# Performance work log

Measured on AMD Instinct MI355X. Metric: run time of the kernel, lower is better.

## Reference

```python
import jax, jax.numpy as jnp
import numpy as np

# sRGB -> XYZ matrix (skimage/CIE, D65 observer 2deg)
_RGB2XYZ = jnp.array([[0.412453, 0.357580, 0.180423],
                      [0.212671, 0.715160, 0.072169],
                      [0.019334, 0.119193, 0.950227]], dtype=jnp.float32)
_WHITE_D65 = jnp.array([0.95047, 1.0, 1.08883], dtype=jnp.float32)


def _srgb_to_linear(c):
    # inverse sRGB gamma
    return jnp.where(c > 0.04045, ((c + 0.055) / 1.055) ** 2.4, c / 12.92)


def _xyz_f(t):
    # CIE Lab nonlinearity
    eps = 0.008856
    return jnp.where(t > eps, jnp.cbrt(t), 7.787 * t + 16.0 / 116.0)


def _rgb2lab(img):
    # img: [..., H, W, 3] sRGB in [0,1]
    lin = _srgb_to_linear(img)
    xyz = jnp.einsum('...c,dc->...d', lin, _RGB2XYZ) / _WHITE_D65
    f = _xyz_f(xyz)
    fx, fy, fz = f[..., 0], f[..., 1], f[..., 2]
    L = 116.0 * fy - 16.0
    a = 500.0 * (fx - fy)
    b = 200.0 * (fy - fz)
    return jnp.stack([L, a, b], axis=-1)


def setup_inputs() -> dict:
    key = jax.random.key(0)
    x = jax.random.uniform(key, (512, 128, 128, 3), dtype=jnp.float32)
    return {"x": x}


def reference(x) -> jnp.ndarray:
    lab = _rgb2lab(x)                       # [B,H,W,3]
    L = lab[..., 0]
    # per-image min-max normalize L channel (reduce over H,W)
    Lmin = jnp.min(L, axis=(1, 2), keepdims=True)
    Lmax = jnp.max(L, axis=(1, 2), keepdims=True)
    L01 = (L - Lmin) / (Lmax - Lmin)
    ab01 = (lab[..., 1:] + 128.0) / 255.0
    out = jnp.concatenate([L01[..., None], ab01], axis=-1)
    return jax.lax.stop_gradient(out).astype(jnp.float32)
```

## Files before the change

### kernel.cpp

```cpp
#include <hip/hip_runtime.h>

#define TPB 1024

typedef __fp16 half2_t __attribute__((ext_vector_type(2)));

__device__ __forceinline__ float fexp2(float x) { return __builtin_amdgcn_exp2f(x); }
__device__ __forceinline__ float flog2(float x) { return __builtin_amdgcn_logf(x); }

__device__ __forceinline__ float s2lin(float c) {
    float p = fexp2(flog2((c + 0.055f) * (1.0f / 1.055f)) * 2.4f);
    float l = c * (1.0f / 12.92f);
    return c > 0.04045f ? p : l;
}

__device__ __forceinline__ float labf(float t) {
    float p = fexp2(flog2(t) * (1.0f / 3.0f));
    float l = 7.787f * t + (16.0f / 116.0f);
    return t > 0.008856f ? p : l;
}

__device__ __forceinline__ void px(float r, float g, float b,
                                   float& L, float& a01, float& b01) {
    float lr = s2lin(r), lg = s2lin(g), lb = s2lin(b);
    float X = 0.43395300f * lr + 0.37621900f * lg + 0.18982460f * lb;
    float Y = 0.21267100f * lr + 0.71516000f * lg + 0.07216900f * lb;
    float Z = 0.01775660f * lr + 0.10946970f * lg + 0.87270740f * lb;
    float fx = labf(X), fy = labf(Y), fz = labf(Z);
    L   = 116.0f * fy - 16.0f;
    a01 = (500.0f * (fx - fy) + 128.0f) * (1.0f / 255.0f);
    b01 = (200.0f * (fy - fz) + 128.0f) * (1.0f / 255.0f);
}

__global__ __launch_bounds__(TPB, 8) void lab_norm_kernel(
        const float* __restrict__ x, float* __restrict__ out) {
    __shared__ float lds[12288];
    __shared__ float smin[16], smax[16];

    const int img = blockIdx.x;
    const size_t ibase = (size_t)img * 49152;
    const int t = threadIdx.x;
    float4* const l4 = (float4*)lds;

    float   Lr[16];
    half2_t AB[16];
    float lmin = 3.4e38f, lmax = -3.4e38f;

#pragma unroll
    for (int g = 0; g < 4; ++g) {
        const float4* __restrict__ in4 = (const float4*)(x + ibase) + g * 3072;
        l4[t]        = in4[t];
        l4[t + 1024] = in4[t + 1024];
        l4[t + 2048] = in4[t + 2048];
        __syncthreads();
#pragma unroll
        for (int j = 0; j < 4; ++j) {
            int p3 = 3 * t + j * 3072;
            float r = lds[p3], gg = lds[p3 + 1], b = lds[p3 + 2];
            float L, a01, b01;
            px(r, gg, b, L, a01, b01);
            lmin = fminf(lmin, L);
            lmax = fmaxf(lmax, L);
            Lr[g * 4 + j] = L;
            AB[g * 4 + j] = __builtin_amdgcn_cvt_pkrtz(a01, b01);
        }
        __syncthreads();
    }

#pragma unroll
    for (int m = 32; m >= 1; m >>= 1) {
        lmin = fminf(lmin, __shfl_xor(lmin, m, 64));
        lmax = fmaxf(lmax, __shfl_xor(lmax, m, 64));
    }
    int wid = t >> 6;
    if ((t & 63) == 0) { smin[wid] = lmin; smax[wid] = lmax; }
    __syncthreads();
    float bmin = smin[0], bmax = smax[0];
#pragma unroll
    for (int i = 1; i < 16; ++i) {
        bmin = fminf(bmin, smin[i]);
        bmax = fmaxf(bmax, smax[i]);
    }
    float s = 1.0f / (bmax - bmin);

#pragma unroll
    for (int g = 0; g < 4; ++g) {
#pragma unroll
        for (int j = 0; j < 4; ++j) {
            int p3 = 3 * t + j * 3072;
            half2_t hv = AB[g * 4 + j];
            lds[p3]     = (Lr[g * 4 + j] - bmin) * s;
            lds[p3 + 1] = (float)hv.x;
            lds[p3 + 2] = (float)hv.y;
        }
        __syncthreads();
        float4* __restrict__ o4 = (float4*)(out + ibase) + g * 3072;
        o4[t]        = l4[t];
        o4[t + 1024] = l4[t + 1024];
        o4[t + 2048] = l4[t + 2048];
        __syncthreads();
    }
}

extern "C" void kernel_launch(void* const* d_in, const int* in_sizes, int n_in,
                              void* d_out, int out_size, void* d_ws, size_t ws_size,
                              hipStream_t stream) {
    (void)in_sizes; (void)n_in; (void)out_size; (void)d_ws; (void)ws_size;
    const float* x = (const float*)d_in[0];
    float* out = (float*)d_out;
    lab_norm_kernel<<<512, TPB, 0, stream>>>(x, out);
}
```

Before: 202.6 us.

## Split into pack and unpack kernels with compact per-pixel workspace encoding

Replaces the single one-block-per-image kernel with two launches of 4096 small blocks, eight per image. The first kernel computes Lab per pixel, records per-block partial min and max of L (max taken as min of 100-L), and packs each pixel into 32 bits: a and b quantized to 8 bits, L stored as fp16. The second kernel combines the partial extrema, unpacks, normalizes L and writes the output. Spreading the work across many more blocks is meant to raise occupancy and memory-level parallelism, at the cost of an extra workspace round trip and lossy quantization of a/b and L. A fallback pair of kernels writes raw output and rescales it in place when the workspace is too small.

```diff
diff --git a/kernel.cpp b/kernel.cpp
--- a/kernel.cpp
+++ b/kernel.cpp
@@ -1,22 +1,18 @@
 #include <hip/hip_runtime.h>
 
-#define TPB 1024
-
-typedef __fp16 half2_t __attribute__((ext_vector_type(2)));
+typedef unsigned int uint32;
 
 __device__ __forceinline__ float fexp2(float x) { return __builtin_amdgcn_exp2f(x); }
 __device__ __forceinline__ float flog2(float x) { return __builtin_amdgcn_logf(x); }
 
 __device__ __forceinline__ float s2lin(float c) {
     float p = fexp2(flog2((c + 0.055f) * (1.0f / 1.055f)) * 2.4f);
-    float l = c * (1.0f / 12.92f);
-    return c > 0.04045f ? p : l;
+    return c > 0.04045f ? p : c * (1.0f / 12.92f);
 }
 
 __device__ __forceinline__ float labf(float t) {
     float p = fexp2(flog2(t) * (1.0f / 3.0f));
-    float l = 7.787f * t + (16.0f / 116.0f);
-    return t > 0.008856f ? p : l;
+    return t > 0.008856f ? p : 7.787f * t + (16.0f / 116.0f);
 }
 
 __device__ __forceinline__ void px(float r, float g, float b,
@@ -31,81 +27,169 @@
     b01 = (200.0f * (fy - fz) + 128.0f) * (1.0f / 255.0f);
 }
 
-__global__ __launch_bounds__(TPB, 8) void lab_norm_kernel(
-        const float* __restrict__ x, float* __restrict__ out) {
-    __shared__ float lds[12288];
-    __shared__ float smin[16], smax[16];
+#define HDR_U32 8192
 
-    const int img = blockIdx.x;
-    const size_t ibase = (size_t)img * 49152;
-    const int t = threadIdx.x;
-    float4* const l4 = (float4*)lds;
+__global__ __launch_bounds__(256) void k1_pack(const float* __restrict__ x,
+                                               uint32* __restrict__ ws) {
+    __shared__ float lds[6144];
+    __shared__ float sm[8];
+    const int b = blockIdx.x, t = threadIdx.x;
+    const int img = b >> 3, sub = b & 7;
+    const size_t P = (size_t)img * 16384 + (size_t)sub * 2048;
+    const float4* __restrict__ in4 =
+        (const float4*)x + (size_t)img * 12288 + (size_t)sub * 1536;
+    float4* l4 = (float4*)lds;
+#pragma unroll
+    for (int j = 0; j < 6; ++j) l4[t + j * 256] = in4[t + j * 256];
+    __syncthreads();
 
-    float   Lr[16];
-    half2_t AB[16];
-    float lmin = 3.4e38f, lmax = -3.4e38f;
+    uint32* __restrict__ wpx = ws + HDR_U32 + P;
+    float m1 = 3.4e38f, m2 = 3.4e38f;
+#pragma unroll
+    for (int j = 0; j < 8; ++j) {
+        int p = t + (j << 8);
+        float L, a01, b01;
+        px(lds[3 * p], lds[3 * p + 1], lds[3 * p + 2], L, a01, b01);
+        m1 = fminf(m1, L);
+        m2 = fminf(m2, 100.0f - L);
+        uint32 au = (uint32)(a01 * 255.0f + 0.5f);
+        uint32 bu = (uint32)(b01 * 255.0f + 0.5f);
+        unsigned short hb = __builtin_bit_cast(unsigned short, (_Float16)L);
+        wpx[p] = au | (bu << 8) | ((uint32)hb << 16);
+    }
+#pragma unroll
+    for (int m = 32; m; m >>= 1) {
+        m1 = fminf(m1, __shfl_xor(m1, m, 64));
+        m2 = fminf(m2, __shfl_xor(m2, m, 64));
+    }
+    if ((t & 63) == 0) { sm[(t >> 6) * 2] = m1; sm[(t >> 6) * 2 + 1] = m2; }
+    __syncthreads();
+    if (t == 0) {
+        float a = fminf(fminf(sm[0], sm[2]), fminf(sm[4], sm[6]));
+        float c = fminf(fminf(sm[1], sm[3]), fminf(sm[5], sm[7]));
+        float* hdr = (float*)ws;
+        hdr[(img * 8 + sub) * 2]     = a;
+        hdr[(img * 8 + sub) * 2 + 1] = c;
+    }
+}
 
+__global__ __launch_bounds__(256) void k2_unpack(const uint32* __restrict__ ws,
+                                                 float* __restrict__ out) {
+    __shared__ float lds[6144];
+    const int b = blockIdx.x, t = threadIdx.x;
+    const int img = b >> 3, sub = b & 7;
+    const size_t P = (size_t)img * 16384 + (size_t)sub * 2048;
+
+    const float* hdr = (const float*)ws + (size_t)img * 16;
+    float Lmin = 3.4e38f, m2 = 3.4e38f;
 #pragma unroll
-    for (int g = 0; g < 4; ++g) {
-        const float4* __restrict__ in4 = (const float4*)(x + ibase) + g * 3072;
-        l4[t]        = in4[t];
-        l4[t + 1024] = in4[t + 1024];
-        l4[t + 2048] = in4[t + 2048];
-        __syncthreads();
+    for (int i = 0; i < 8; ++i) {
+        Lmin = fminf(Lmin, hdr[2 * i]);
+        m2   = fminf(m2, hdr[2 * i + 1]);
+    }
+    float s = 1.0f / ((100.0f - m2) - Lmin);
+
+    const uint32* __restrict__ wpx = ws + HDR_U32 + P;
 #pragma unroll
-        for (int j = 0; j < 4; ++j) {
-            int p3 = 3 * t + j * 3072;
-            float r = lds[p3], gg = lds[p3 + 1], b = lds[p3 + 2];
-            float L, a01, b01;
-            px(r, gg, b, L, a01, b01);
-            lmin = fminf(lmin, L);
-            lmax = fmaxf(lmax, L);
-            Lr[g * 4 + j] = L;
-            AB[g * 4 + j] = __builtin_amdgcn_cvt_pkrtz(a01, b01);
-        }
-        __syncthreads();
+    for (int j = 0; j < 8; ++j) {
+        int p = t + (j << 8);
+        uint32 v = wpx[p];
+        float a01 = (float)(v & 255u) * (1.0f / 255.0f);
+        float b01 = (float)((v >> 8) & 255u) * (1.0f / 255.0f);
+        float L = (float)__builtin_bit_cast(_Float16, (unsigned short)(v >> 16));
+        lds[3 * p]     = (L - Lmin) * s;
+        lds[3 * p + 1] = a01;
+        lds[3 * p + 2] = b01;
     }
+    __syncthreads();
+    float4* l4 = (float4*)lds;
+    float4* __restrict__ o4 =
+        (float4*)out + (size_t)img * 12288 + (size_t)sub * 1536;
+#pragma unroll
+    for (int j = 0; j < 6; ++j) o4[t + j * 256] = l4[t + j * 256];
+}
 
+__global__ __launch_bounds__(256) void k1_raw(const float* __restrict__ x,
+                                              float* __restrict__ out,
+                                              float* __restrict__ hdr) {
+    __shared__ float lds[6144];
+    __shared__ float sm[8];
+    const int b = blockIdx.x, t = threadIdx.x;
+    const int img = b >> 3, sub = b & 7;
+    const float4* __restrict__ in4 =
+        (const float4*)x + (size_t)img * 12288 + (size_t)sub * 1536;
+    float4* l4 = (float4*)lds;
 #pragma unroll
-    for (int m = 32; m >= 1; m >>= 1) {
-        lmin = fminf(lmin, __shfl_xor(lmin, m, 64));
-        lmax = fmaxf(lmax, __shfl_xor(lmax, m, 64));
+    for (int j = 0; j < 6; ++j) l4[t + j * 256] = in4[t + j * 256];
+    __syncthreads();
+    float m1 = 3.4e38f, m2 = 3.4e38f;
+#pragma unroll
+    for (int j = 0; j < 8; ++j) {
+        int p = t + (j << 8);
+        float L, a01, b01;
+        px(lds[3 * p], lds[3 * p + 1], lds[3 * p + 2], L, a01, b01);
+        m1 = fminf(m1, L);
+        m2 = fminf(m2, 100.0f - L);
+        lds[3 * p] = L; lds[3 * p + 1] = a01; lds[3 * p + 2] = b01;
     }
-    int wid = t >> 6;
-    if ((t & 63) == 0) { smin[wid] = lmin; smax[wid] = lmax; }
     __syncthreads();
-    float bmin = smin[0], bmax = smax[0];
+    float4* __restrict__ o4 =
+        (float4*)out + (size_t)img * 12288 + (size_t)sub * 1536;
 #pragma unroll
-    for (int i = 1; i < 16; ++i) {
-        bmin = fminf(bmin, smin[i]);
-        bmax = fmaxf(bmax, smax[i]);
+    for (int j = 0; j < 6; ++j) o4[t + j * 256] = l4[t + j * 256];
+#pragma unroll
+    for (int m = 32; m; m >>= 1) {
+        m1 = fminf(m1, __shfl_xor(m1, m, 64));
+        m2 = fminf(m2, __shfl_xor(m2, m, 64));
     }
-    float s = 1.0f / (bmax - bmin);
+    if ((t & 63) == 0) { sm[(t >> 6) * 2] = m1; sm[(t >> 6) * 2 + 1] = m2; }
+    __syncthreads();
+    if (t == 0) {
+        hdr[(img * 8 + sub) * 2] =
+            fminf(fminf(sm[0], sm[2]), fminf(sm[4], sm[6]));
+        hdr[(img * 8 + sub) * 2 + 1] =
+            fminf(fminf(sm[1], sm[3]), fminf(sm[5], sm[7]));
+    }
+}
 
+__global__ __launch_bounds__(256) void k2_rescale(float* __restrict__ out,
+                                                  const float* __restrict__ hdr0) {
+    const int b = blockIdx.x, t = threadIdx.x;
+    const int img = b >> 3, sub = b & 7;
+    const float* hdr = hdr0 + (size_t)img * 16;
+    float Lmin = 3.4e38f, m2 = 3.4e38f;
 #pragma unroll
-    for (int g = 0; g < 4; ++g) {
+    for (int i = 0; i < 8; ++i) {
+        Lmin = fminf(Lmin, hdr[2 * i]);
+        m2   = fminf(m2, hdr[2 * i + 1]);
+    }
+    float s = 1.0f / ((100.0f - m2) - Lmin);
+    float4* __restrict__ o4 =
+        (float4*)out + (size_t)img * 12288 + (size_t)sub * 1536;
 #pragma unroll
-        for (int j = 0; j < 4; ++j) {
-            int p3 = 3 * t + j * 3072;
-            half2_t hv = AB[g * 4 + j];
-            lds[p3]     = (Lr[g * 4 + j] - bmin) * s;
-            lds[p3 + 1] = (float)hv.x;
-            lds[p3 + 2] = (float)hv.y;
-        }
-        __syncthreads();
-        float4* __restrict__ o4 = (float4*)(out + ibase) + g * 3072;
-        o4[t]        = l4[t];
-        o4[t + 1024] = l4[t + 1024];
-        o4[t + 2048] = l4[t + 2048];
-        __syncthreads();
+    for (int j = 0; j < 6; ++j) {
+        int idx = t + j * 256;
+        float4 v = o4[idx];
+        int r = idx % 3;
+        if (r == 0)      { v.x = (v.x - Lmin) * s; v.w = (v.w - Lmin) * s; }
+        else if (r == 1) { v.z = (v.z - Lmin) * s; }
+        else             { v.y = (v.y - Lmin) * s; }
+        o4[idx] = v;
     }
 }
 
 extern "C" void kernel_launch(void* const* d_in, const int* in_sizes, int n_in,
                               void* d_out, int out_size, void* d_ws, size_t ws_size,
                               hipStream_t stream) {
-    (void)in_sizes; (void)n_in; (void)out_size; (void)d_ws; (void)ws_size;
+    (void)in_sizes; (void)n_in; (void)out_size;
     const float* x = (const float*)d_in[0];
     float* out = (float*)d_out;
-    lab_norm_kernel<<<512, TPB, 0, stream>>>(x, out);
+    const size_t need = 32768ull + 512ull * 16384ull * 4ull;
+    if (ws_size >= need) {
+        k1_pack<<<4096, 256, 0, stream>>>(x, (uint32*)d_ws);
+        k2_unpack<<<4096, 256, 0, stream>>>((const uint32*)d_ws, out);
+    } else {
+        k1_raw<<<4096, 256, 0, stream>>>(x, out, (float*)d_ws);
+        k2_rescale<<<4096, 256, 0, stream>>>(out, (const float*)d_ws);
+    }
 }
```

New measurement: 186.6 us. 1.09x faster.
